# Optimization experiments

Hardware: AMD Instinct MI355X
Metric: run time of the kernel (lower is better)

Reference implementation:

```python
import jax, jax.numpy as jnp
import numpy as np
import math

N_HEAD = 16
ROPE_BASE = 10000.0


def _rope(x):
    # x: [B, S, H, Dh]
    S, d = x.shape[1], x.shape[-1]
    inv_freq = 1.0 / (ROPE_BASE ** (jnp.arange(0, d, 2, dtype=jnp.float32) / d))
    t = jnp.arange(S, dtype=jnp.float32)
    freqs = jnp.einsum('i,j->ij', t, inv_freq)              # [S, d/2]
    emb = jnp.concatenate([freqs, freqs], axis=-1)          # [S, d]
    cos = jnp.cos(emb)[None, :, None, :]
    sin = jnp.sin(emb)[None, :, None, :]
    x1, x2 = jnp.split(x, 2, axis=-1)
    x_rot = jnp.concatenate([-x2, x1], axis=-1)
    return x * cos + x_rot * sin


def setup_inputs() -> dict:
    key = jax.random.key(0)
    ks = jax.random.split(key, 6)
    B, S, D = 2, 2048, 1024
    x = jax.random.normal(ks[0], (B, S, D), dtype=jnp.float32)
    w = lambda k: jax.random.normal(k, (D, D), dtype=jnp.float32) * 0.02
    return {'x': x, 'wq': w(ks[1]), 'wk': w(ks[2]), 'wv': w(ks[3]),
            'wg': w(ks[4]), 'wo': w(ks[5])}


def reference(x, wq, wk, wv, wg, wo):
    B, S, D = x.shape
    H = N_HEAD
    Dh = D // H

    # projections (torch Linear: y = x @ W^T)
    q = (x @ wq.T).reshape(B, S, H, Dh)
    k = (x @ wk.T).reshape(B, S, H, Dh)
    v = (x @ wv.T).reshape(B, S, H, Dh)

    q = _rope(q)
    k = _rope(k)

    q = q.transpose(0, 2, 1, 3)  # [B,H,S,Dh]
    k = k.transpose(0, 2, 1, 3)
    v = v.transpose(0, 2, 1, 3)

    # per-head exponential decay mask (causal)
    idx = jnp.arange(S)
    d_mask = jnp.tril(idx[:, None] - idx[None, :]).astype(jnp.float32)  # [S,S]
    gamma = 1.0 - jnp.exp2(-5.0 - jnp.arange(H, dtype=jnp.float32))     # [H]
    causal = jnp.tril(jnp.ones((S, S), dtype=jnp.float32))
    decay_matrix = jnp.power(gamma[:, None, None], d_mask) * causal     # [H,S,S]

    retention = jnp.einsum('bhsd,bhtd->bhst', q, k) / math.sqrt(Dh)
    retention = retention * decay_matrix[None]                          # [B,H,S,S]

    out = jnp.einsum('bhst,bhtd->bhsd', retention, v)
    out = out.transpose(0, 2, 1, 3).reshape(B, S, D)

    g = jax.nn.silu(x @ wg.T)
    return (out * g) @ wo.T
```

## Files before the change

kernel.cpp:

```cpp
#include <hip/hip_runtime.h>
#include <hip/hip_bf16.h>

typedef unsigned short u16;
typedef unsigned int u32;
typedef __attribute__((ext_vector_type(8))) short short8;
typedef __attribute__((ext_vector_type(4))) float f32x4;

#define S_LEN 2048
#define D_DIM 1024
#define NH    16
#define DH    64
#define B_SZ  2
#define M_ROWS (B_SZ * S_LEN)
#define NCHUNK (S_LEN / 64)

__device__ __forceinline__ u16 f2bf(float f) {
  u32 u = __float_as_uint(f);
  u += 0x7FFFu + ((u >> 16) & 1u);
  return (u16)(u >> 16);
}
__device__ __forceinline__ float bf2f(u16 u) {
  return __uint_as_float(((u32)u) << 16);
}
__device__ __forceinline__ u32 pack_bf2(float lo, float hi) {
  __hip_bfloat162 p = __float22bfloat162_rn(make_float2(lo, hi));
  u32 r;
  __builtin_memcpy(&r, &p, 4);
  return r;
}

__device__ __forceinline__ void gll16(const void* g, void* l) {
  __builtin_amdgcn_global_load_lds((const __attribute__((address_space(1))) u32*)g,
                                   (__attribute__((address_space(3))) u32*)l,
                                   16, 0, 0);
}

__global__ __launch_bounds__(256) void cvt_bf16(const float* __restrict__ src,
                                                u16* __restrict__ dst, int n4) {
  int i = blockIdx.x * 256 + threadIdx.x;
  if (i >= n4) return;
  const float4 v = ((const float4*)src)[i];
  u32 lo = (u32)f2bf(v.x) | ((u32)f2bf(v.y) << 16);
  u32 hi = (u32)f2bf(v.z) | ((u32)f2bf(v.w) << 16);
  ((u32*)dst)[2 * i]     = lo;
  ((u32*)dst)[2 * i + 1] = hi;
}

__global__ __launch_bounds__(256) void cvt_w5(const float* __restrict__ wq,
                                              const float* __restrict__ wk,
                                              const float* __restrict__ wv,
                                              const float* __restrict__ wg,
                                              const float* __restrict__ wo,
                                              u16* __restrict__ dst) {
  const int seg = blockIdx.y;
  const float* src = seg == 0 ? wq : seg == 1 ? wk : seg == 2 ? wv : seg == 3 ? wg : wo;
  const int i = blockIdx.x * 256 + threadIdx.x;
  const float4 v = ((const float4*)src)[i];
  u32* d = (u32*)(dst + (size_t)seg * D_DIM * D_DIM);
  d[2 * i]     = (u32)f2bf(v.x) | ((u32)f2bf(v.y) << 16);
  d[2 * i + 1] = (u32)f2bf(v.z) | ((u32)f2bf(v.w) << 16);
}

__global__ __launch_bounds__(256) void rope_tab(float2* __restrict__ tab) {
  int i = blockIdx.x * 256 + threadIdx.x;
  int s = i >> 5, j = i & 31;
  float inv = exp2f(-(float)j * (13.287712379549449f / 32.f));
  float fr = (float)s * inv;
  tab[i] = make_float2(cosf(fr), sinf(fr));
}

template<int BM, int BN, int WPM, int WPN>
__device__ __forceinline__ void gemm_bk32(const u16* __restrict__ A,
                                          const u16* __restrict__ W,
                                          const int m0, const int n0,
                                          u16* lds,
                                          f32x4 (&acc)[BM / (WPM * 16)][BN / (WPN * 16)])
{
  constexpr int T   = WPM * WPN * 64;
  constexpr int MR  = BM / (WPM * 16);
  constexpr int NR  = BN / (WPN * 16);
  constexpr int ALD = BM * 32;
  constexpr int BLD = BN * 32;
  constexpr int BUF = ALD + BLD;
  constexpr int NK  = D_DIM / 32;

  const int tid  = threadIdx.x;
  const int lane = tid & 63, wid = tid >> 6;
  const int wm = wid / WPN, wn = wid % WPN;
  const int l15 = lane & 15, l4 = lane >> 4;

  #pragma unroll
  for (int m = 0; m < MR; ++m)
    #pragma unroll
    for (int n = 0; n < NR; ++n)
      acc[m][n] = (f32x4){0.f, 0.f, 0.f, 0.f};

  auto stage = [&](int kt) {
    const int k0 = kt * 32;
    u16* la = lds + (kt & 3) * BUF;
    u16* lb = la + ALD;
    #pragma unroll
    for (int j = 0; j < BM * 4 / T; ++j) {
      const int c = tid + j * T;
      gll16(A + (size_t)(m0 + (c >> 2)) * D_DIM + k0 + (c & 3) * 8, la + c * 8);
    }
    #pragma unroll
    for (int j = 0; j < BN * 4 / T; ++j) {
      const int c = tid + j * T;
      gll16(W + (size_t)(n0 + (c >> 2)) * D_DIM + k0 + (c & 3) * 8, lb + c * 8);
    }
  };

  stage(0);
  stage(1);
  asm volatile("s_waitcnt vmcnt(4)" ::: "memory");
  __builtin_amdgcn_s_barrier();
  __builtin_amdgcn_sched_barrier(0);

  for (int i = 0; i < NK; ++i) {
    if (i + 2 < NK) stage(i + 2);
    const u16* la = lds + (i & 3) * BUF + (wm * (BM / WPM) + l15) * 32 + l4 * 8;
    const u16* lb = lds + (i & 3) * BUF + ALD + (wn * (BN / WPN) + l15) * 32 + l4 * 8;
    short8 av[MR], bv[NR];
    #pragma unroll
    for (int m = 0; m < MR; ++m) av[m] = *(const short8*)(la + m * 16 * 32);
    #pragma unroll
    for (int n = 0; n < NR; ++n) bv[n] = *(const short8*)(lb + n * 16 * 32);
    __builtin_amdgcn_s_setprio(1);
    #pragma unroll
    for (int m = 0; m < MR; ++m)
      #pragma unroll
      for (int n = 0; n < NR; ++n)
        acc[m][n] = __builtin_amdgcn_mfma_f32_16x16x32_bf16(av[m], bv[n], acc[m][n], 0, 0, 0);
    __builtin_amdgcn_s_setprio(0);
    if (i + 2 < NK) asm volatile("s_waitcnt vmcnt(4)" ::: "memory");
    else            asm volatile("s_waitcnt vmcnt(0)" ::: "memory");
    __builtin_amdgcn_s_barrier();
    __builtin_amdgcn_sched_barrier(0);
  }
}

__global__ __launch_bounds__(512, 2) void proj_kernel(
    const u16* __restrict__ xb, const u16* __restrict__ wcat,
    u16* __restrict__ qb, u16* __restrict__ kb, u16* __restrict__ kT,
    u16* __restrict__ vT, u16* __restrict__ gb,
    const float2* __restrict__ rope)
{
  __shared__ u16 lds[4 * (256 * 32 + 256 * 32)];
  f32x4 acc[8][4];
  const int m0 = blockIdx.y * 256, n0 = blockIdx.x * 256;
  gemm_bk32<256, 256, 2, 4>(xb, wcat, m0, n0, lds, acc);

  const int lane = threadIdx.x & 63, wid = threadIdx.x >> 6;
  const int wm = wid >> 2, wn = wid & 3;
  const int l15 = lane & 15, l4 = lane >> 4;
  const int gcol = n0 + wn * 64;
  const int z  = gcol >> 10;
  const int hh = (gcol >> 6) & (NH - 1);
  const int mcol = gcol & (D_DIM - 1);
  const int rbase = m0 + wm * 128 + l4 * 4;
  const float lgh = log2f(1.f - exp2f(-5.f - (float)hh));

  if (z <= 1) {
    u16* dst = z ? kb : qb;
    const float slg  = z ? -lgh : lgh;
    const float base = z ? 1.f : 0.125f;
    #pragma unroll
    for (int m = 0; m < 8; ++m) {
      float o1v[2][4], o2v[2][4];
      #pragma unroll
      for (int r = 0; r < 4; ++r) {
        const int row = rbase + m * 16 + r;
        const int s = row & (S_LEN - 1);
        const float sc = base * exp2f((float)(s & 63) * slg);
        #pragma unroll
        for (int n = 0; n < 2; ++n) {
          const int dh0 = n * 16 + l15;
          const float2 cs = rope[s * 32 + dh0];
          const float x1 = acc[m][n][r], x2 = acc[m][n + 2][r];
          const float o1 = (x1 * cs.x - x2 * cs.y) * sc;
          const float o2 = (x2 * cs.x + x1 * cs.y) * sc;
          dst[(size_t)row * D_DIM + mcol + n * 16 + l15]       = f2bf(o1);
          dst[(size_t)row * D_DIM + mcol + (n + 2) * 16 + l15] = f2bf(o2);
          o1v[n][r] = o1; o2v[n][r] = o2;
        }
      }
      if (z == 1) {
        const int row0 = rbase + m * 16;
        const int bb = row0 >> 11, sr = row0 & (S_LEN - 1);
        #pragma unroll
        for (int n = 0; n < 2; ++n) {
          const int dh0 = n * 16 + l15;
          const uint2 p1 = make_uint2(pack_bf2(o1v[n][0], o1v[n][1]), pack_bf2(o1v[n][2], o1v[n][3]));
          const uint2 p2 = make_uint2(pack_bf2(o2v[n][0], o2v[n][1]), pack_bf2(o2v[n][2], o2v[n][3]));
          *(uint2*)(kT + (size_t)((bb * NH + hh) * DH + dh0) * S_LEN + sr)      = p1;
          *(uint2*)(kT + (size_t)((bb * NH + hh) * DH + dh0 + 32) * S_LEN + sr) = p2;
        }
      }
    }
  } else if (z == 2) {
    #pragma unroll
    for (int m = 0; m < 8; ++m) {
      const int row0 = rbase + m * 16;
      const int bb = row0 >> 11, sr = row0 & (S_LEN - 1);
      #pragma unroll
      for (int n = 0; n < 4; ++n) {
        const int dh = n * 16 + l15;
        const uint2 p = make_uint2(pack_bf2(acc[m][n][0], acc[m][n][1]),
                                   pack_bf2(acc[m][n][2], acc[m][n][3]));
        *(uint2*)(vT + (size_t)((bb * NH + hh) * DH + dh) * S_LEN + sr) = p;
      }
    }
  } else {
    #pragma unroll
    for (int m = 0; m < 8; ++m)
      #pragma unroll
      for (int n = 0; n < 4; ++n)
        #pragma unroll
        for (int r = 0; r < 4; ++r) {
          const int row = rbase + m * 16 + r;
          const float v = acc[m][n][r];
          gb[(size_t)row * D_DIM + mcol + n * 16 + l15] = f2bf(v / (1.f + __expf(-v)));
        }
  }
}

__global__ __launch_bounds__(256) void chunk_accum(
    const u16* __restrict__ kT, const u16* __restrict__ vT,
    u16* __restrict__ At)
{
  const int tid = threadIdx.x, lane = tid & 63, w = tid >> 6;
  const int l15 = lane & 15, l4 = lane >> 4;
  const int bh = blockIdx.x >> 5, c = blockIdx.x & 31;

  short8 a[2], bfr[2][4];
  #pragma unroll
  for (int kk = 0; kk < 2; ++kk) {
    a[kk] = *(const short8*)(vT + (size_t)(bh * DH + w * 16 + l15) * S_LEN + c * 64 + kk * 32 + l4 * 8);
    #pragma unroll
    for (int n = 0; n < 4; ++n)
      bfr[kk][n] = *(const short8*)(kT + (size_t)(bh * DH + n * 16 + l15) * S_LEN + c * 64 + kk * 32 + l4 * 8);
  }
  f32x4 acc[4];
  #pragma unroll
  for (int n = 0; n < 4; ++n) acc[n] = (f32x4){0.f, 0.f, 0.f, 0.f};
  #pragma unroll
  for (int kk = 0; kk < 2; ++kk)
    #pragma unroll
    for (int n = 0; n < 4; ++n)
      acc[n] = __builtin_amdgcn_mfma_f32_16x16x32_bf16(a[kk], bfr[kk][n], acc[n], 0, 0, 0);

  u16* dst = At + ((size_t)(bh * NCHUNK + c)) * 4096;
  #pragma unroll
  for (int n = 0; n < 4; ++n)
    #pragma unroll
    for (int r = 0; r < 4; ++r)
      dst[(w * 16 + l4 * 4 + r) * 64 + n * 16 + l15] = f2bf(acc[n][r]);
}

__global__ __launch_bounds__(256) void chunk_scan(
    const u16* __restrict__ At, u16* __restrict__ St)
{
  const int gid = blockIdx.x * 256 + threadIdx.x;
  const int bh = gid >> 12, e = gid & 4095;
  const int h = bh & (NH - 1);
  const float lg = log2f(1.f - exp2f(-5.f - (float)h));
  const float gC = exp2f(64.f * lg);
  const u16* src = At + (size_t)bh * NCHUNK * 4096 + e;
  u16* dst = St + (size_t)bh * NCHUNK * 4096 + e;
  float s = 0.f;
  for (int c = 0; c < NCHUNK; ++c) {
    const float a = bf2f(src[(size_t)c * 4096]);
    dst[(size_t)c * 4096] = f2bf(s);
    s = gC * (s + a);
  }
}

__global__ __launch_bounds__(256) void chunk_out(
    const u16* __restrict__ qb, const u16* __restrict__ kb,
    const u16* __restrict__ vT, const u16* __restrict__ St,
    const u16* __restrict__ gb, u16* __restrict__ ob)
{
  __shared__ u16 Ps[4][16 * 64];

  const int tid = threadIdx.x, lane = tid & 63, w = tid >> 6;
  const int l15 = lane & 15, l4 = lane >> 4;
  const int bh = blockIdx.x >> 5, c = blockIdx.x & 31;
  const int b = bh >> 4, h = bh & (NH - 1);
  const int q0 = c * 64 + w * 16;

  short8 qfr[2], kf[2][4], vf[2][4], sf[2][4];
  #pragma unroll
  for (int kk = 0; kk < 2; ++kk) {
    qfr[kk] = *(const short8*)(qb + (size_t)(b * S_LEN + q0 + l15) * D_DIM + h * DH + kk * 32 + l4 * 8);
    #pragma unroll
    for (int t = 0; t < 4; ++t)
      kf[kk][t] = *(const short8*)(kb + (size_t)(b * S_LEN + c * 64 + t * 16 + l15) * D_DIM + h * DH + kk * 32 + l4 * 8);
    #pragma unroll
    for (int n = 0; n < 4; ++n) {
      vf[kk][n] = *(const short8*)(vT + (size_t)(bh * DH + n * 16 + l15) * S_LEN + c * 64 + kk * 32 + l4 * 8);
      sf[kk][n] = *(const short8*)(St + ((size_t)(bh * NCHUNK + c)) * 4096 + (n * 16 + l15) * 64 + kk * 32 + l4 * 8);
    }
  }

  f32x4 st[4];
  #pragma unroll
  for (int tf = 0; tf < 4; ++tf) st[tf] = (f32x4){0.f, 0.f, 0.f, 0.f};
  #pragma unroll
  for (int kk = 0; kk < 2; ++kk)
    #pragma unroll
    for (int tf = 0; tf < 4; ++tf)
      st[tf] = __builtin_amdgcn_mfma_f32_16x16x32_bf16(kf[kk][tf], qfr[kk], st[tf], 0, 0, 0);

  f32x4 acc[4];
  #pragma unroll
  for (int n = 0; n < 4; ++n) acc[n] = (f32x4){0.f, 0.f, 0.f, 0.f};
  #pragma unroll
  for (int kk = 0; kk < 2; ++kk)
    #pragma unroll
    for (int n = 0; n < 4; ++n)
      acc[n] = __builtin_amdgcn_mfma_f32_16x16x32_bf16(qfr[kk], sf[kk][n], acc[n], 0, 0, 0);

  u16* const psw = &Ps[w][0];
  const int qq = w * 16 + l15;
  #pragma unroll
  for (int tf = 0; tf < 4; ++tf) {
    const int tb = tf * 16 + l4 * 4;
    const float v0 = (tb + 0 <= qq) ? st[tf][0] : 0.f;
    const float v1 = (tb + 1 <= qq) ? st[tf][1] : 0.f;
    const float v2 = (tb + 2 <= qq) ? st[tf][2] : 0.f;
    const float v3 = (tb + 3 <= qq) ? st[tf][3] : 0.f;
    const uint2 u = make_uint2(pack_bf2(v0, v1), pack_bf2(v2, v3));
    const int boff = l15 * 128 + ((tf * 32 + l4 * 8) ^ ((l15 & 7) << 4));
    *(uint2*)((char*)psw + boff) = u;
  }

  #pragma unroll
  for (int kk = 0; kk < 2; ++kk) {
    const int boff = l15 * 128 + ((kk * 64 + l4 * 16) ^ ((l15 & 7) << 4));
    const short8 pa = *(const short8*)((const char*)psw + boff);
    #pragma unroll
    for (int n = 0; n < 4; ++n)
      acc[n] = __builtin_amdgcn_mfma_f32_16x16x32_bf16(pa, vf[kk][n], acc[n], 0, 0, 0);
  }

  #pragma unroll
  for (int n = 0; n < 4; ++n)
    #pragma unroll
    for (int r = 0; r < 4; ++r) {
      const size_t idx = (size_t)(b * S_LEN + q0 + l4 * 4 + r) * D_DIM + h * DH + n * 16 + l15;
      ob[idx] = f2bf(acc[n][r] * bf2f(gb[idx]));
    }
}

__global__ __launch_bounds__(256, 2) void final_kernel(
    const u16* __restrict__ ob, const u16* __restrict__ wob,
    float* __restrict__ out)
{
  __shared__ u16 lds[4 * (128 * 32 + 128 * 32)];
  f32x4 acc[4][4];
  const int m0 = blockIdx.y * 128, n0 = blockIdx.x * 128;
  gemm_bk32<128, 128, 2, 2>(ob, wob, m0, n0, lds, acc);

  const int lane = threadIdx.x & 63, wid = threadIdx.x >> 6;
  const int wm = wid >> 1, wn = wid & 1;
  const int rbase = m0 + wm * 64 + (lane >> 4) * 4;
  const int cbase = n0 + wn * 64 + (lane & 15);
  #pragma unroll
  for (int m = 0; m < 4; ++m)
    #pragma unroll
    for (int n = 0; n < 4; ++n)
      #pragma unroll
      for (int r = 0; r < 4; ++r)
        out[(size_t)(rbase + m * 16 + r) * D_DIM + cbase + n * 16] = acc[m][n][r];
}

extern "C" void kernel_launch(void* const* d_in, const int* in_sizes, int n_in,
                              void* d_out, int out_size, void* d_ws, size_t ws_size,
                              hipStream_t stream) {
  (void)in_sizes; (void)n_in; (void)out_size; (void)ws_size;
  const float* x  = (const float*)d_in[0];
  const float* wq = (const float*)d_in[1];
  const float* wk = (const float*)d_in[2];
  const float* wv = (const float*)d_in[3];
  const float* wg = (const float*)d_in[4];
  const float* wo = (const float*)d_in[5];
  float* out = (float*)d_out;

  char* ws = (char*)d_ws;
  const size_t SZ_X = (size_t)M_ROWS * D_DIM * 2;
  const size_t SZ_W = (size_t)D_DIM * D_DIM * 2;
  u16* xb   = (u16*)(ws);
  u16* wcat = (u16*)(ws + SZ_X);
  u16* wob  = (u16*)(ws + SZ_X + 4 * SZ_W);
  u16* qb   = (u16*)(ws + 1 * SZ_X + 5 * SZ_W);
  u16* kb   = (u16*)(ws + 2 * SZ_X + 5 * SZ_W);
  u16* vT   = (u16*)(ws + 3 * SZ_X + 5 * SZ_W);
  u16* gb   = (u16*)(ws + 4 * SZ_X + 5 * SZ_W);
  u16* kT   = (u16*)(ws + 5 * SZ_X + 5 * SZ_W);
  u16* ob   = kT;
  float2* rope = (float2*)(ws + 6 * SZ_X + 5 * SZ_W);
  u16* St   = (u16*)(ws);
  u16* At   = (u16*)(ws + SZ_X);

  const int nx4 = M_ROWS * D_DIM / 4;
  const int nw4 = D_DIM * D_DIM / 4;
  cvt_bf16<<<nx4 / 256, 256, 0, stream>>>(x, xb, nx4);
  cvt_w5<<<dim3(nw4 / 256, 5), 256, 0, stream>>>(wq, wk, wv, wg, wo, wcat);
  rope_tab<<<(S_LEN * 32) / 256, 256, 0, stream>>>(rope);

  proj_kernel<<<dim3(16, 16), 512, 0, stream>>>(xb, wcat, qb, kb, kT, vT, gb, rope);

  chunk_accum<<<dim3(B_SZ * NH * NCHUNK), 256, 0, stream>>>(kT, vT, At);
  chunk_scan<<<dim3(B_SZ * NH * 4096 / 256), 256, 0, stream>>>(At, St);
  chunk_out<<<dim3(B_SZ * NH * NCHUNK), 256, 0, stream>>>(qb, kb, vT, St, gb, ob);

  final_kernel<<<dim3(D_DIM / 128, M_ROWS / 128), 256, 0, stream>>>(ob, wob, out);
}
```

Before: 110.2 us.

## Rewrite projection GEMM with BK64 swizzled LDS, ping-pong schedule, fused prep

The projection GEMM gets a new main loop. It uses K-tiles of 64 stored in LDS with an XOR swizzle to avoid bank conflicts, a double-buffered half-tile staging plan interleaved with quarter-tile MFMA groups, and barriers plus setprio to overlap loads with compute. The three prep kernels (x conversion, weight conversion, rope table) are merged into one launch to cut launch overhead. Block indices for both GEMMs are remapped with a swizzle to improve L2 reuse. The hand-written schedule adds many barriers and relies on exact waitcnt counts, so it risks stalls or ordering errors.

```diff
diff --git a/kernel.cpp b/kernel.cpp
--- a/kernel.cpp
+++ b/kernel.cpp
@@ -35,108 +35,41 @@
                                    16, 0, 0);
 }
 
-__global__ __launch_bounds__(256) void cvt_bf16(const float* __restrict__ src,
-                                                u16* __restrict__ dst, int n4) {
-  int i = blockIdx.x * 256 + threadIdx.x;
-  if (i >= n4) return;
-  const float4 v = ((const float4*)src)[i];
-  u32 lo = (u32)f2bf(v.x) | ((u32)f2bf(v.y) << 16);
-  u32 hi = (u32)f2bf(v.z) | ((u32)f2bf(v.w) << 16);
-  ((u32*)dst)[2 * i]     = lo;
-  ((u32*)dst)[2 * i + 1] = hi;
-}
-
-__global__ __launch_bounds__(256) void cvt_w5(const float* __restrict__ wq,
-                                              const float* __restrict__ wk,
-                                              const float* __restrict__ wv,
-                                              const float* __restrict__ wg,
-                                              const float* __restrict__ wo,
-                                              u16* __restrict__ dst) {
-  const int seg = blockIdx.y;
-  const float* src = seg == 0 ? wq : seg == 1 ? wk : seg == 2 ? wv : seg == 3 ? wg : wo;
-  const int i = blockIdx.x * 256 + threadIdx.x;
-  const float4 v = ((const float4*)src)[i];
-  u32* d = (u32*)(dst + (size_t)seg * D_DIM * D_DIM);
-  d[2 * i]     = (u32)f2bf(v.x) | ((u32)f2bf(v.y) << 16);
-  d[2 * i + 1] = (u32)f2bf(v.z) | ((u32)f2bf(v.w) << 16);
-}
-
-__global__ __launch_bounds__(256) void rope_tab(float2* __restrict__ tab) {
-  int i = blockIdx.x * 256 + threadIdx.x;
-  int s = i >> 5, j = i & 31;
-  float inv = exp2f(-(float)j * (13.287712379549449f / 32.f));
-  float fr = (float)s * inv;
-  tab[i] = make_float2(cosf(fr), sinf(fr));
-}
-
-template<int BM, int BN, int WPM, int WPN>
-__device__ __forceinline__ void gemm_bk32(const u16* __restrict__ A,
-                                          const u16* __restrict__ W,
-                                          const int m0, const int n0,
-                                          u16* lds,
-                                          f32x4 (&acc)[BM / (WPM * 16)][BN / (WPN * 16)])
-{
-  constexpr int T   = WPM * WPN * 64;
-  constexpr int MR  = BM / (WPM * 16);
-  constexpr int NR  = BN / (WPN * 16);
-  constexpr int ALD = BM * 32;
-  constexpr int BLD = BN * 32;
-  constexpr int BUF = ALD + BLD;
-  constexpr int NK  = D_DIM / 32;
-
-  const int tid  = threadIdx.x;
-  const int lane = tid & 63, wid = tid >> 6;
-  const int wm = wid / WPN, wn = wid % WPN;
-  const int l15 = lane & 15, l4 = lane >> 4;
-
-  #pragma unroll
-  for (int m = 0; m < MR; ++m)
-    #pragma unroll
-    for (int n = 0; n < NR; ++n)
-      acc[m][n] = (f32x4){0.f, 0.f, 0.f, 0.f};
-
-  auto stage = [&](int kt) {
-    const int k0 = kt * 32;
-    u16* la = lds + (kt & 3) * BUF;
-    u16* lb = la + ALD;
-    #pragma unroll
-    for (int j = 0; j < BM * 4 / T; ++j) {
-      const int c = tid + j * T;
-      gll16(A + (size_t)(m0 + (c >> 2)) * D_DIM + k0 + (c & 3) * 8, la + c * 8);
-    }
-    #pragma unroll
-    for (int j = 0; j < BN * 4 / T; ++j) {
-      const int c = tid + j * T;
-      gll16(W + (size_t)(n0 + (c >> 2)) * D_DIM + k0 + (c & 3) * 8, lb + c * 8);
-    }
-  };
-
-  stage(0);
-  stage(1);
-  asm volatile("s_waitcnt vmcnt(4)" ::: "memory");
-  __builtin_amdgcn_s_barrier();
-  __builtin_amdgcn_sched_barrier(0);
-
-  for (int i = 0; i < NK; ++i) {
-    if (i + 2 < NK) stage(i + 2);
-    const u16* la = lds + (i & 3) * BUF + (wm * (BM / WPM) + l15) * 32 + l4 * 8;
-    const u16* lb = lds + (i & 3) * BUF + ALD + (wn * (BN / WPN) + l15) * 32 + l4 * 8;
-    short8 av[MR], bv[NR];
-    #pragma unroll
-    for (int m = 0; m < MR; ++m) av[m] = *(const short8*)(la + m * 16 * 32);
-    #pragma unroll
-    for (int n = 0; n < NR; ++n) bv[n] = *(const short8*)(lb + n * 16 * 32);
-    __builtin_amdgcn_s_setprio(1);
-    #pragma unroll
-    for (int m = 0; m < MR; ++m)
-      #pragma unroll
-      for (int n = 0; n < NR; ++n)
-        acc[m][n] = __builtin_amdgcn_mfma_f32_16x16x32_bf16(av[m], bv[n], acc[m][n], 0, 0, 0);
-    __builtin_amdgcn_s_setprio(0);
-    if (i + 2 < NK) asm volatile("s_waitcnt vmcnt(4)" ::: "memory");
-    else            asm volatile("s_waitcnt vmcnt(0)" ::: "memory");
-    __builtin_amdgcn_s_barrier();
-    __builtin_amdgcn_sched_barrier(0);
+#define SP1() __builtin_amdgcn_s_setprio(1)
+#define SP0() __builtin_amdgcn_s_setprio(0)
+#define BAR() __builtin_amdgcn_s_barrier()
+#define LGKM0() do { asm volatile("s_waitcnt lgkmcnt(0)" ::: "memory"); \
+                     __builtin_amdgcn_sched_barrier(0); } while (0)
+
+__global__ __launch_bounds__(256) void prep_kernel(
+    const float* __restrict__ x,
+    const float* __restrict__ wq, const float* __restrict__ wk,
+    const float* __restrict__ wv, const float* __restrict__ wg,
+    const float* __restrict__ wo,
+    u16* __restrict__ xb, u16* __restrict__ wcat, float2* __restrict__ rope)
+{
+  const int bid = blockIdx.x, tid = threadIdx.x;
+  if (bid < 4096) {
+    const int i = bid * 256 + tid;
+    const float4 v = ((const float4*)x)[i];
+    u32* d = (u32*)xb;
+    d[2 * i]     = (u32)f2bf(v.x) | ((u32)f2bf(v.y) << 16);
+    d[2 * i + 1] = (u32)f2bf(v.z) | ((u32)f2bf(v.w) << 16);
+  } else if (bid < 9216) {
+    const int t = bid - 4096;
+    const int seg = t >> 10;
+    const float* src = seg == 0 ? wq : seg == 1 ? wk : seg == 2 ? wv : seg == 3 ? wg : wo;
+    const int i = (t & 1023) * 256 + tid;
+    const float4 v = ((const float4*)src)[i];
+    u32* d = (u32*)(wcat + (size_t)seg * D_DIM * D_DIM);
+    d[2 * i]     = (u32)f2bf(v.x) | ((u32)f2bf(v.y) << 16);
+    d[2 * i + 1] = (u32)f2bf(v.z) | ((u32)f2bf(v.w) << 16);
+  } else {
+    const int i = (bid - 9216) * 256 + tid;
+    const int s = i >> 5, j = i & 31;
+    float inv = exp2f(-(float)j * (13.287712379549449f / 32.f));
+    float fr = (float)s * inv;
+    rope[i] = make_float2(cosf(fr), sinf(fr));
   }
 }
 
@@ -146,16 +79,128 @@
     u16* __restrict__ vT, u16* __restrict__ gb,
     const float2* __restrict__ rope)
 {
-  __shared__ u16 lds[4 * (256 * 32 + 256 * 32)];
-  f32x4 acc[8][4];
-  const int m0 = blockIdx.y * 256, n0 = blockIdx.x * 256;
-  gemm_bk32<256, 256, 2, 4>(xb, wcat, m0, n0, lds, acc);
-
-  const int lane = threadIdx.x & 63, wid = threadIdx.x >> 6;
+  __shared__ u16 lds[65536];
+  const int tid = threadIdx.x, lane = tid & 63, wid = tid >> 6;
   const int wm = wid >> 2, wn = wid & 3;
   const int l15 = lane & 15, l4 = lane >> 4;
+
+  const int bid = blockIdx.x;
+  const int sw = (bid & 7) * 32 + (bid >> 3);
+  const int m0 = (sw & 15) * 256;
+  const int n0 = (sw >> 4) * 256;
+
+  f32x4 acc[8][4];
+  #pragma unroll
+  for (int m = 0; m < 8; ++m)
+    #pragma unroll
+    for (int n = 0; n < 4; ++n)
+      acc[m][n] = (f32x4){0.f, 0.f, 0.f, 0.f};
+
+  short8 a[4][2], b0[2][2], b1[2][2];
+
+  auto stA = [&](int t, int h) {
+    u16* dst = lds + ((t & 1) * 2 + h) * 8192;
+    const u16* src = xb + (size_t)(m0 + h * 128) * D_DIM + t * 64;
+    #pragma unroll
+    for (int j = 0; j < 2; ++j) {
+      const int c = tid + j * 512, row = c >> 3, ch = c & 7;
+      gll16(src + (size_t)row * D_DIM + ((ch ^ (row & 7)) << 3), dst + c * 8);
+    }
+  };
+  auto stB = [&](int t, int h) {
+    u16* dst = lds + 32768 + ((t & 1) * 2 + h) * 8192;
+    const u16* src = wcat + (size_t)(n0 + h * 128) * D_DIM + t * 64;
+    #pragma unroll
+    for (int j = 0; j < 2; ++j) {
+      const int c = tid + j * 512, row = c >> 3, ch = c & 7;
+      gll16(src + (size_t)row * D_DIM + ((ch ^ (row & 7)) << 3), dst + c * 8);
+    }
+  };
+  auto ldA = [&](int d, int mh) {
+    const u16* base = lds + (d * 2 + wm) * 8192;
+    #pragma unroll
+    for (int m = 0; m < 4; ++m) {
+      const int lr = mh * 64 + m * 16 + l15;
+      #pragma unroll
+      for (int kk = 0; kk < 2; ++kk)
+        a[m][kk] = *(const short8*)(base + lr * 64 + (((kk * 4 + l4) ^ (lr & 7)) << 3));
+    }
+  };
+  auto ldB = [&](short8 (&b)[2][2], int d, int nh) {
+    const u16* base = lds + 32768 + (d * 2 + (wn >> 1)) * 8192;
+    #pragma unroll
+    for (int j = 0; j < 2; ++j) {
+      const int lr = (wn & 1) * 64 + (nh * 2 + j) * 16 + l15;
+      #pragma unroll
+      for (int kk = 0; kk < 2; ++kk)
+        b[j][kk] = *(const short8*)(base + lr * 64 + (((kk * 4 + l4) ^ (lr & 7)) << 3));
+    }
+  };
+  auto quad = [&](int mh, int nh, short8 (&b)[2][2]) {
+    #pragma unroll
+    for (int m = 0; m < 4; ++m)
+      #pragma unroll
+      for (int j = 0; j < 2; ++j)
+        #pragma unroll
+        for (int kk = 0; kk < 2; ++kk)
+          acc[mh * 4 + m][nh * 2 + j] =
+              __builtin_amdgcn_mfma_f32_16x16x32_bf16(a[m][kk], b[j][kk],
+                                                      acc[mh * 4 + m][nh * 2 + j], 0, 0, 0);
+  };
+
+  stB(0, 0); stA(0, 0); stB(0, 1); stA(0, 1); stB(1, 0); stB(1, 1);
+  asm volatile("s_waitcnt vmcnt(4)" ::: "memory");
+  BAR();
+
+  for (int i = 0; i < 8; ++i) {
+    const int t1 = 2 * i + 1, t2 = 2 * i + 2, t3 = 2 * i + 3;
+    ldA(0, 0); ldB(b0, 0, 0);
+    stA(t1, 0);
+    asm volatile("s_waitcnt lgkmcnt(8)" ::: "memory");
+    BAR(); LGKM0();
+    SP1(); quad(0, 0, b0); SP0();
+    BAR();
+    ldB(b1, 0, 1);
+    stA(t1, 1);
+    BAR(); LGKM0();
+    SP1(); quad(0, 1, b1); SP0();
+    BAR();
+    ldA(0, 1);
+    if (t2 < 16) stB(t2, 0);
+    BAR(); LGKM0();
+    SP1(); quad(1, 0, b0); SP0();
+    BAR();
+    if (t2 < 16) stA(t2, 0);
+    BAR(); LGKM0();
+    SP1(); quad(1, 1, b1); SP0();
+    if (i == 7) asm volatile("s_waitcnt vmcnt(0)" ::: "memory");
+    else        asm volatile("s_waitcnt vmcnt(4)" ::: "memory");
+    BAR();
+    ldA(1, 0); ldB(b0, 1, 0);
+    if (t2 < 16) stB(t2, 1);
+    asm volatile("s_waitcnt lgkmcnt(8)" ::: "memory");
+    BAR(); LGKM0();
+    SP1(); quad(0, 0, b0); SP0();
+    BAR();
+    ldB(b1, 1, 1);
+    if (t2 < 16) stA(t2, 1);
+    BAR(); LGKM0();
+    SP1(); quad(0, 1, b1); SP0();
+    BAR();
+    ldA(1, 1);
+    if (t3 < 16) stB(t3, 0);
+    BAR(); LGKM0();
+    SP1(); quad(1, 0, b0); SP0();
+    BAR();
+    if (t3 < 16) stB(t3, 1);
+    BAR(); LGKM0();
+    SP1(); quad(1, 1, b1); SP0();
+    if (i < 7) asm volatile("s_waitcnt vmcnt(4)" ::: "memory");
+    BAR();
+  }
+
   const int gcol = n0 + wn * 64;
-  const int z  = gcol >> 10;
+  const int z = gcol >> 10;
   const int hh = (gcol >> 6) & (NH - 1);
   const int mcol = gcol & (D_DIM - 1);
   const int rbase = m0 + wm * 128 + l4 * 4;
@@ -225,6 +270,77 @@
   }
 }
 
+template<int BM, int BN, int WPM, int WPN>
+__device__ __forceinline__ void gemm_bk32(const u16* __restrict__ A,
+                                          const u16* __restrict__ W,
+                                          const int m0, const int n0,
+                                          u16* lds,
+                                          f32x4 (&acc)[BM / (WPM * 16)][BN / (WPN * 16)])
+{
+  constexpr int T   = WPM * WPN * 64;
+  constexpr int MR  = BM / (WPM * 16);
+  constexpr int NR  = BN / (WPN * 16);
+  constexpr int ALD = BM * 32;
+  constexpr int BLD = BN * 32;
+  constexpr int BUF = ALD + BLD;
+  constexpr int NK  = D_DIM / 32;
+
+  const int tid  = threadIdx.x;
+  const int lane = tid & 63, wid = tid >> 6;
+  const int wm = wid / WPN, wn = wid % WPN;
+  const int l15 = lane & 15, l4 = lane >> 4;
+
+  #pragma unroll
+  for (int m = 0; m < MR; ++m)
+    #pragma unroll
+    for (int n = 0; n < NR; ++n)
+      acc[m][n] = (f32x4){0.f, 0.f, 0.f, 0.f};
+
+  auto stage = [&](int kt) {
+    const int k0 = kt * 32;
+    u16* la = lds + (kt & 3) * BUF;
+    u16* lb = la + ALD;
+    #pragma unroll
+    for (int j = 0; j < BM * 4 / T; ++j) {
+      const int c = tid + j * T;
+      gll16(A + (size_t)(m0 + (c >> 2)) * D_DIM + k0 + (c & 3) * 8, la + c * 8);
+    }
+    #pragma unroll
+    for (int j = 0; j < BN * 4 / T; ++j) {
+      const int c = tid + j * T;
+      gll16(W + (size_t)(n0 + (c >> 2)) * D_DIM + k0 + (c & 3) * 8, lb + c * 8);
+    }
+  };
+
+  stage(0);
+  stage(1);
+  asm volatile("s_waitcnt vmcnt(4)" ::: "memory");
+  BAR();
+  __builtin_amdgcn_sched_barrier(0);
+
+  for (int i = 0; i < NK; ++i) {
+    if (i + 2 < NK) stage(i + 2);
+    const u16* la = lds + (i & 3) * BUF + (wm * (BM / WPM) + l15) * 32 + l4 * 8;
+    const u16* lb = lds + (i & 3) * BUF + ALD + (wn * (BN / WPN) + l15) * 32 + l4 * 8;
+    short8 av[MR], bv[NR];
+    #pragma unroll
+    for (int m = 0; m < MR; ++m) av[m] = *(const short8*)(la + m * 16 * 32);
+    #pragma unroll
+    for (int n = 0; n < NR; ++n) bv[n] = *(const short8*)(lb + n * 16 * 32);
+    SP1();
+    #pragma unroll
+    for (int m = 0; m < MR; ++m)
+      #pragma unroll
+      for (int n = 0; n < NR; ++n)
+        acc[m][n] = __builtin_amdgcn_mfma_f32_16x16x32_bf16(av[m], bv[n], acc[m][n], 0, 0, 0);
+    SP0();
+    if (i + 2 < NK) asm volatile("s_waitcnt vmcnt(4)" ::: "memory");
+    else            asm volatile("s_waitcnt vmcnt(0)" ::: "memory");
+    BAR();
+    __builtin_amdgcn_sched_barrier(0);
+  }
+}
+
 __global__ __launch_bounds__(256) void chunk_accum(
     const u16* __restrict__ kT, const u16* __restrict__ vT,
     u16* __restrict__ At)
@@ -359,7 +475,10 @@
 {
   __shared__ u16 lds[4 * (128 * 32 + 128 * 32)];
   f32x4 acc[4][4];
-  const int m0 = blockIdx.y * 128, n0 = blockIdx.x * 128;
+  const int bid = blockIdx.x;
+  const int sw = (bid & 7) * 32 + (bid >> 3);
+  const int n0 = (sw & 7) * 128;
+  const int m0 = (sw >> 3) * 128;
   gemm_bk32<128, 128, 2, 2>(ob, wob, m0, n0, lds, acc);
 
   const int lane = threadIdx.x & 63, wid = threadIdx.x >> 6;
@@ -403,17 +522,13 @@
   u16* St   = (u16*)(ws);
   u16* At   = (u16*)(ws + SZ_X);
 
-  const int nx4 = M_ROWS * D_DIM / 4;
-  const int nw4 = D_DIM * D_DIM / 4;
-  cvt_bf16<<<nx4 / 256, 256, 0, stream>>>(x, xb, nx4);
-  cvt_w5<<<dim3(nw4 / 256, 5), 256, 0, stream>>>(wq, wk, wv, wg, wo, wcat);
-  rope_tab<<<(S_LEN * 32) / 256, 256, 0, stream>>>(rope);
-
-  proj_kernel<<<dim3(16, 16), 512, 0, stream>>>(xb, wcat, qb, kb, kT, vT, gb, rope);
+  prep_kernel<<<dim3(9472), 256, 0, stream>>>(x, wq, wk, wv, wg, wo, xb, wcat, rope);
+
+  proj_kernel<<<dim3(256), 512, 0, stream>>>(xb, wcat, qb, kb, kT, vT, gb, rope);
 
   chunk_accum<<<dim3(B_SZ * NH * NCHUNK), 256, 0, stream>>>(kT, vT, At);
   chunk_scan<<<dim3(B_SZ * NH * 4096 / 256), 256, 0, stream>>>(At, St);
   chunk_out<<<dim3(B_SZ * NH * NCHUNK), 256, 0, stream>>>(qb, kb, vT, St, gb, ob);
 
-  final_kernel<<<dim3(D_DIM / 128, M_ROWS / 128), 256, 0, stream>>>(ob, wob, out);
-}
+  final_kernel<<<dim3(256), 256, 0, stream>>>(ob, wob, out);
+}
```

Result: faster. 102.5 us (-6.9%).
